# Kernel optimization log

Hardware: AMD Instinct MI355X
Metric: run time of the kernel (lower is better)

Reference implementation:

```python
import jax, jax.numpy as jnp
import numpy as np

EMBED = 256
HEADS = 8
HEAD_DIM = EMBED // HEADS
LEVELS = 4
POINTS = 4
QUERY_DIM = 128
NQ = QUERY_DIM * QUERY_DIM
HIDDEN = 512
CHANNELS = [24, 40, 112, 1280]
SHAPES = [(64, 64), (32, 32), (16, 16), (8, 8)]
EPS = 1e-5


def group_norm(x, g, b, groups=32, eps=EPS):
    B, C, H, W = x.shape
    xr = x.reshape(B, groups, C // groups, H, W)
    mu = xr.mean(axis=(2, 3, 4), keepdims=True)
    var = xr.var(axis=(2, 3, 4), keepdims=True)
    xn = ((xr - mu) / jnp.sqrt(var + eps)).reshape(B, C, H, W)
    return xn * g[:, None, None] + b[:, None, None]


def layer_norm(x, g, b, eps=EPS):
    mu = x.mean(-1, keepdims=True)
    var = x.var(-1, keepdims=True)
    return (x - mu) / jnp.sqrt(var + eps) * g + b


def _sample_level(v, loc):
    # v: (B, H8, hd, H, W) value for one level; loc: (B, nq, H8, P, 2) in [0,1]
    B, Hh, hd, H, W = v.shape
    nq, P = loc.shape[1], loc.shape[3]
    # grid_sample semantics, align_corners=False, zero padding
    x = loc[..., 0] * W - 0.5
    y = loc[..., 1] * H - 0.5
    x0 = jnp.floor(x)
    y0 = jnp.floor(y)
    dx = x - x0
    dy = y - y0
    x0i = x0.astype(jnp.int32)
    y0i = y0.astype(jnp.int32)
    vflat = v.reshape(B, Hh, hd, H * W)

    def gather(xi, yi):
        valid = ((xi >= 0) & (xi < W) & (yi >= 0) & (yi < H)).astype(v.dtype)
        idx = jnp.clip(yi, 0, H - 1) * W + jnp.clip(xi, 0, W - 1)
        idxr = idx.transpose(0, 2, 1, 3).reshape(B, Hh, 1, nq * P)
        g = jnp.take_along_axis(vflat, idxr, axis=3).reshape(B, Hh, hd, nq, P)
        return g * valid.transpose(0, 2, 1, 3)[:, :, None]

    g00 = gather(x0i, y0i)
    g01 = gather(x0i + 1, y0i)
    g10 = gather(x0i, y0i + 1)
    g11 = gather(x0i + 1, y0i + 1)
    wx = dx.transpose(0, 2, 1, 3)[:, :, None]  # (B,H8,1,nq,P)
    wy = dy.transpose(0, 2, 1, 3)[:, :, None]
    return g00 * (1 - wx) * (1 - wy) + g01 * wx * (1 - wy) + g10 * (1 - wx) * wy + g11 * wx * wy


def reference(Q, grd0, grd1, grd2, grd3, batch_size,
              proj_w0, proj_b0, gn_g0, gn_b0,
              proj_w1, proj_b1, gn_g1, gn_b1,
              proj_w2, proj_b2, gn_g2, gn_b2,
              proj_w3, proj_b3, gn_g3, gn_b3,
              value_w, value_b, off_w, off_b, attw_w, attw_b,
              out_w, out_b, lin1_w, lin1_b, lin2_w, lin2_b, ln_g, ln_b):
    grd = [grd0, grd1, grd2, grd3]
    proj_w = [proj_w0, proj_w1, proj_w2, proj_w3]
    proj_b = [proj_b0, proj_b1, proj_b2, proj_b3]
    gn_g = [gn_g0, gn_g1, gn_g2, gn_g3]
    gn_b = [gn_b0, gn_b1, gn_b2, gn_b3]

    B = Q.shape[0]
    # project each level to embed dims (1x1 conv + GroupNorm) and flatten
    feats = []
    for l in range(LEVELS):
        f = jnp.einsum('bchw,co->bohw', grd[l], proj_w[l]) + proj_b[l][:, None, None]
        f = group_norm(f, gn_g[l], gn_b[l])
        feats.append(f.reshape(B, EMBED, -1).transpose(0, 2, 1))  # (B, H*W, E)
    value = jnp.concatenate(feats, axis=1)  # (B, NV, E)

    # reference points: meshgrid 'xy' over linspace(0,1,query_dim), shape (1,nq,1,2)
    lin = jnp.linspace(0.0, 1.0, QUERY_DIM)
    gx, gy = jnp.meshgrid(lin, lin, indexing='xy')
    ref = jnp.stack([gx, gy], axis=-1).reshape(1, NQ, 1, 2)

    # MSDeformAttn (mmcv): value proj, sampling offsets, attention weights
    v = (value @ value_w + value_b).reshape(B, -1, HEADS, HEAD_DIM)
    offs = (Q @ off_w + off_b).reshape(B, NQ, HEADS, LEVELS, POINTS, 2)
    aw = (Q @ attw_w + attw_b).reshape(B, NQ, HEADS, LEVELS * POINTS)
    aw = jax.nn.softmax(aw, axis=-1).reshape(B, NQ, HEADS, LEVELS, POINTS)

    # offset normalizer: (W, H) per level
    norm = jnp.array([[w, h] for (h, w) in SHAPES], dtype=Q.dtype)  # (L,2)
    # sampling_locations: (B,nq,H8,L,P,2); ref broadcasts over heads/levels/points
    loc = ref[:, :, None, :, None, :] + offs / norm[None, None, None, :, None, :]

    starts = np.concatenate([[0], np.cumsum([h * w for h, w in SHAPES])])
    out = jnp.zeros((B, HEADS, HEAD_DIM, NQ), dtype=Q.dtype)
    for l, (H, W) in enumerate(SHAPES):
        vl = v[:, starts[l]:starts[l + 1]].transpose(0, 2, 3, 1).reshape(B, HEADS, HEAD_DIM, H, W)
        sampled = _sample_level(vl, loc[:, :, :, l])  # (B,H8,hd,nq,P)
        out = out + jnp.einsum('bhdqp,bqhp->bhdq', sampled, aw[:, :, :, l])
    attn = out.transpose(0, 3, 1, 2).reshape(B, NQ, EMBED)
    attn = attn @ out_w + out_b
    attn = attn + Q  # mmcv internal residual (dropout is identity in eval)

    fused = attn + Q
    ffn = layer_norm(jax.nn.relu(fused @ lin1_w + lin1_b) @ lin2_w + lin2_b, ln_g, ln_b)
    return fused + ffn


def setup_inputs() -> dict:
    key = jax.random.key(0)
    ks = jax.random.split(key, 40)
    B = 4
    d = {
        'Q': jax.random.normal(ks[0], (B, NQ, EMBED), jnp.float32),
        'grd0': jax.random.normal(ks[1], (B, 24, 64, 64), jnp.float32),
        'grd1': jax.random.normal(ks[2], (B, 40, 32, 32), jnp.float32),
        'grd2': jax.random.normal(ks[3], (B, 112, 16, 16), jnp.float32),
        'grd3': jax.random.normal(ks[4], (B, 1280, 8, 8), jnp.float32),
        'batch_size': B,
    }
    i = 5
    for l, c in enumerate(CHANNELS):
        d[f'proj_w{l}'] = jax.random.normal(ks[i], (c, EMBED), jnp.float32) * (1.0 / np.sqrt(c)); i += 1
        d[f'proj_b{l}'] = jnp.zeros((EMBED,), jnp.float32)
        d[f'gn_g{l}'] = jnp.ones((EMBED,), jnp.float32)
        d[f'gn_b{l}'] = jnp.zeros((EMBED,), jnp.float32)

    def lin(k, fin, fout, scale=1.0):
        return jax.random.normal(k, (fin, fout), jnp.float32) * (scale / np.sqrt(fin))

    d['value_w'] = lin(ks[i], EMBED, EMBED); i += 1
    d['value_b'] = jnp.zeros((EMBED,), jnp.float32)
    d['off_w'] = lin(ks[i], EMBED, HEADS * LEVELS * POINTS * 2, 0.1); i += 1
    d['off_b'] = jnp.zeros((HEADS * LEVELS * POINTS * 2,), jnp.float32)
    d['attw_w'] = lin(ks[i], EMBED, HEADS * LEVELS * POINTS); i += 1
    d['attw_b'] = jnp.zeros((HEADS * LEVELS * POINTS,), jnp.float32)
    d['out_w'] = lin(ks[i], EMBED, EMBED); i += 1
    d['out_b'] = jnp.zeros((EMBED,), jnp.float32)
    d['lin1_w'] = lin(ks[i], EMBED, HIDDEN); i += 1
    d['lin1_b'] = jnp.zeros((HIDDEN,), jnp.float32)
    d['lin2_w'] = lin(ks[i], HIDDEN, EMBED); i += 1
    d['lin2_b'] = jnp.zeros((EMBED,), jnp.float32)
    d['ln_g'] = jnp.ones((EMBED,), jnp.float32)
    d['ln_b'] = jnp.zeros((EMBED,), jnp.float32)
    return d
```

## Files before the change

### kernel.cpp

```cpp
#include <hip/hip_runtime.h>
#include <hip/hip_bf16.h>


#define NQc 16384
#define NVc 5440

typedef __attribute__((ext_vector_type(8))) short short8;
typedef __attribute__((ext_vector_type(4))) short short4v;
typedef __attribute__((ext_vector_type(4))) float f32x4;

#define GLOAD16(gp, lp)                                                        \
  __builtin_amdgcn_global_load_lds(                                           \
      (const __attribute__((address_space(1))) unsigned int*)(gp),            \
      (__attribute__((address_space(3))) unsigned int*)(lp), 16, 0, 0)

__device__ __forceinline__ float wred(float v) {
#pragma unroll
  for (int o = 32; o > 0; o >>= 1) v += __shfl_down(v, o);
  return v;
}

__global__ __launch_bounds__(256) void tcast_kernel(
    const float* __restrict__ w, __hip_bfloat16* __restrict__ wt, int K, int N) {
  int i = blockIdx.x * 256 + threadIdx.x;
  if (i < K * N) {
    int k = i / N, n = i - k * N;
    wt[(size_t)n * K + k] = __float2bfloat16(w[i]);
  }
}

__global__ __launch_bounds__(256) void tcast_pad_kernel(
    const float* __restrict__ w, __hip_bfloat16* __restrict__ wt,
    int K, int Kp, int N) {
  int i = blockIdx.x * 256 + threadIdx.x;
  if (i < N * Kp) {
    int n = i / Kp, k = i - n * Kp;
    wt[i] = (k < K) ? __float2bfloat16(w[k * N + n]) : __float2bfloat16(0.f);
  }
}

__global__ __launch_bounds__(256) void tpad_kernel(
    const float* __restrict__ grd, __hip_bfloat16* __restrict__ xp,
    int C, int Kp, int HW, int total) {
  const int i = blockIdx.x * 256 + threadIdx.x;
  if (i >= total) return;
  const int row = i / Kp;
  const int k = i - row * Kp;
  const int b = row / HW;
  const int hw = row - b * HW;
  xp[i] = (k < C) ? __float2bfloat16(grd[((size_t)b * C + k) * HW + hw])
                  : __float2bfloat16(0.f);
}

__global__ __launch_bounds__(256) void gn_kernel(
    const float* __restrict__ val, __hip_bfloat16* __restrict__ valb,
    const float* __restrict__ gg0, const float* __restrict__ gb0,
    const float* __restrict__ gg1, const float* __restrict__ gb1,
    const float* __restrict__ gg2, const float* __restrict__ gb2,
    const float* __restrict__ gg3, const float* __restrict__ gb3) {
  const int bid = blockIdx.x;
  const int grp = bid & 31;
  const int l = (bid >> 5) & 3;
  const int b = bid >> 7;
  int HW, startB; const float *gg, *gbeta;
  if (l == 0)      { HW = 4096; startB = 0;     gg = gg0; gbeta = gb0; }
  else if (l == 1) { HW = 1024; startB = 16384; gg = gg1; gbeta = gb1; }
  else if (l == 2) { HW = 256;  startB = 20480; gg = gg2; gbeta = gb2; }
  else             { HW = 64;   startB = 21504; gg = gg3; gbeta = gb3; }
  const int n = HW * 8;
  const size_t base = ((size_t)(startB + b * HW)) * 256 + grp * 8;
  float s = 0.f, s2 = 0.f;
  for (int i = threadIdx.x; i < n; i += 256) {
    float x = val[base + (size_t)(i >> 3) * 256 + (i & 7)];
    s += x; s2 += x * x;
  }
  s = wred(s); s2 = wred(s2);
  __shared__ float red[8];
  const int wv = threadIdx.x >> 6;
  if ((threadIdx.x & 63) == 0) { red[wv] = s; red[4 + wv] = s2; }
  __syncthreads();
  const float S = red[0] + red[1] + red[2] + red[3];
  const float S2 = red[4] + red[5] + red[6] + red[7];
  const float inv_n = 1.f / (float)n;
  const float mu = S * inv_n;
  const float var = S2 * inv_n - mu * mu;
  const float rstd = rsqrtf(var + 1e-5f);
  for (int i = threadIdx.x; i < n; i += 256) {
    const int j = i & 7;
    const int e = grp * 8 + j;
    const size_t idx = base + (size_t)(i >> 3) * 256 + j;
    const float y = (val[idx] - mu) * rstd * gg[e] + gbeta[e];
    valb[idx] = __float2bfloat16(y);
  }
}

template <int MODE, bool XF32>
__global__ __launch_bounds__(256) void gemm_bt(
    const void* __restrict__ Xv, const __hip_bfloat16* __restrict__ Wt,
    const float* __restrict__ bias, float* __restrict__ Cf,
    __hip_bfloat16* __restrict__ Cb, const float* __restrict__ Qres,
    int M, int N, int K) {
  const int m0 = blockIdx.x * 128;
  const int n0 = blockIdx.y * 128;
  const int tid = threadIdx.x;
  const int wave = tid >> 6;
  const int lane = tid & 63;
  const int wm = wave >> 1;
  const int wn = wave & 1;
  const int l15 = lane & 15;
  const int l4 = lane >> 4;
  __shared__ __align__(16) __hip_bfloat16 As[128 * 64];
  __shared__ __align__(16) __hip_bfloat16 Bs[128 * 64];
  f32x4 acc[4][4];
#pragma unroll
  for (int m = 0; m < 4; ++m)
#pragma unroll
    for (int n = 0; n < 4; ++n) acc[m][n] = (f32x4){0.f, 0.f, 0.f, 0.f};

  for (int k0 = 0; k0 < K; k0 += 64) {
#pragma unroll
    for (int j = 0; j < 4; ++j) {
      const int e = (j * 256 + tid) * 8;
      const int r = e >> 6;
      const int k = e & 63;
      if constexpr (XF32) {
        const float* Xf = (const float*)Xv;
        const float4 a = *reinterpret_cast<const float4*>(&Xf[(size_t)(m0 + r) * K + k0 + k]);
        const float4 b = *reinterpret_cast<const float4*>(&Xf[(size_t)(m0 + r) * K + k0 + k + 4]);
        union { __hip_bfloat16 h[8]; short8 v; } u;
        u.h[0] = __float2bfloat16(a.x); u.h[1] = __float2bfloat16(a.y);
        u.h[2] = __float2bfloat16(a.z); u.h[3] = __float2bfloat16(a.w);
        u.h[4] = __float2bfloat16(b.x); u.h[5] = __float2bfloat16(b.y);
        u.h[6] = __float2bfloat16(b.z); u.h[7] = __float2bfloat16(b.w);
        *reinterpret_cast<short8*>(&As[e]) = u.v;
        *reinterpret_cast<short8*>(&Bs[e]) =
            *reinterpret_cast<const short8*>(&Wt[(size_t)(n0 + r) * K + k0 + k]);
      } else {
        const __hip_bfloat16* Xb = (const __hip_bfloat16*)Xv;
        GLOAD16(&Xb[(size_t)(m0 + r) * K + k0 + k], &As[e]);
        GLOAD16(&Wt[(size_t)(n0 + r) * K + k0 + k], &Bs[e]);
      }
    }
    __syncthreads();
#pragma unroll
    for (int ks = 0; ks < 2; ++ks) {
      short8 a[4], bfr[4];
#pragma unroll
      for (int m = 0; m < 4; ++m)
        a[m] = *reinterpret_cast<const short8*>(
            &As[(wm * 64 + m * 16 + l15) * 64 + ks * 32 + l4 * 8]);
#pragma unroll
      for (int n = 0; n < 4; ++n)
        bfr[n] = *reinterpret_cast<const short8*>(
            &Bs[(wn * 64 + n * 16 + l15) * 64 + ks * 32 + l4 * 8]);
#pragma unroll
      for (int m = 0; m < 4; ++m)
#pragma unroll
        for (int n = 0; n < 4; ++n)
          acc[m][n] = __builtin_amdgcn_mfma_f32_16x16x32_bf16(a[m], bfr[n], acc[m][n], 0, 0, 0);
    }
    __syncthreads();
  }

#pragma unroll
  for (int m = 0; m < 4; ++m) {
    const int row0 = m0 + wm * 64 + m * 16 + l4 * 4;
#pragma unroll
    for (int n = 0; n < 4; ++n) {
      const int col = n0 + wn * 64 + n * 16 + l15;
      const float bv = bias[col];
#pragma unroll
      for (int r = 0; r < 4; ++r) {
        const size_t ci = (size_t)(row0 + r) * N + col;
        float f = acc[m][n][r] + bv;
        if (MODE == 0) {
          Cf[ci] = f;
        } else if (MODE == 1) {
          Cb[ci] = __float2bfloat16(fmaxf(f, 0.f));
        } else if (MODE == 2) {
          f += 2.f * Qres[ci];
          Cf[ci] = f;
          Cb[ci] = __float2bfloat16(f);
        } else {
          Cb[ci] = __float2bfloat16(f);
        }
      }
    }
  }
}

__global__ __launch_bounds__(256) void softmax_kernel(float* __restrict__ aw) {
  const size_t t = (size_t)blockIdx.x * 256 + threadIdx.x;
  float* p = aw + t * 16;
  float v[16];
  *reinterpret_cast<float4*>(&v[0])  = *reinterpret_cast<const float4*>(p + 0);
  *reinterpret_cast<float4*>(&v[4])  = *reinterpret_cast<const float4*>(p + 4);
  *reinterpret_cast<float4*>(&v[8])  = *reinterpret_cast<const float4*>(p + 8);
  *reinterpret_cast<float4*>(&v[12]) = *reinterpret_cast<const float4*>(p + 12);
  float mx = v[0];
#pragma unroll
  for (int j = 1; j < 16; ++j) mx = fmaxf(mx, v[j]);
  float sum = 0.f;
#pragma unroll
  for (int j = 0; j < 16; ++j) { v[j] = __expf(v[j] - mx); sum += v[j]; }
  const float inv = 1.f / sum;
#pragma unroll
  for (int j = 0; j < 16; ++j) v[j] *= inv;
  *reinterpret_cast<float4*>(p + 0)  = *reinterpret_cast<const float4*>(&v[0]);
  *reinterpret_cast<float4*>(p + 4)  = *reinterpret_cast<const float4*>(&v[4]);
  *reinterpret_cast<float4*>(p + 8)  = *reinterpret_cast<const float4*>(&v[8]);
  *reinterpret_cast<float4*>(p + 12) = *reinterpret_cast<const float4*>(&v[12]);
}

__global__ __launch_bounds__(256) void sampler_kernel(
    const float* __restrict__ V, const float* __restrict__ OFFS,
    const float* __restrict__ AW, __hip_bfloat16* __restrict__ ATT) {
  __shared__ int   sIdx[512 * 4];
  __shared__ float sW[512 * 4];
  const int blk = blockIdx.x;
  const int b = blk >> 12;
  const int q0 = (blk & 4095) << 2;
  const int bid0 = blk << 2;

  for (int j = threadIdx.x; j < 512; j += 256) {
    const int q   = j >> 7;
    const int h   = (j >> 4) & 7;
    const int tap = j & 15;
    const int l = tap >> 2;
    const int gq = bid0 + q;
    const int qq = q0 + q;
    const float rx = (float)(qq & 127) * (1.f / 127.f);
    const float ry = (float)(qq >> 7) * (1.f / 127.f);
    const float2 oxy = *reinterpret_cast<const float2*>(
        &OFFS[(size_t)gq * 256 + h * 32 + tap * 2]);
    const float aw = AW[(size_t)gq * 128 + h * 16 + tap];
    const int W = 64 >> l;
    const int HWl = W * W;
    const int startB = (l == 0) ? 0 : (l == 1) ? 16384 : (l == 2) ? 20480 : 21504;
    const int rowbase = startB + b * HWl;
    const float fW = (float)W;
    const float x = rx * fW + oxy.x - 0.5f;
    const float y = ry * fW + oxy.y - 0.5f;
    const float x0f = floorf(x);
    const float y0f = floorf(y);
    const int x0 = (int)x0f;
    const int y0 = (int)y0f;
    const float dx = x - x0f;
    const float dy = y - y0f;
    const int x1 = x0 + 1, y1 = y0 + 1;
    const float mx0 = (x0 >= 0 && x0 < W) ? 1.f : 0.f;
    const float mx1 = (x1 >= 0 && x1 < W) ? 1.f : 0.f;
    const float my0 = (y0 >= 0 && y0 < W) ? 1.f : 0.f;
    const float my1 = (y1 >= 0 && y1 < W) ? 1.f : 0.f;
    const int x0c = min(max(x0, 0), W - 1);
    const int x1c = min(max(x1, 0), W - 1);
    const int y0c = min(max(y0, 0), W - 1);
    const int y1c = min(max(y1, 0), W - 1);
    int4 I;
    I.x = rowbase + y0c * W + x0c;
    I.y = rowbase + y0c * W + x1c;
    I.z = rowbase + y1c * W + x0c;
    I.w = rowbase + y1c * W + x1c;
    float4 Wv;
    Wv.x = aw * (1.f - dx) * (1.f - dy) * (mx0 * my0);
    Wv.y = aw * dx * (1.f - dy) * (mx1 * my0);
    Wv.z = aw * (1.f - dx) * dy * (mx0 * my1);
    Wv.w = aw * dx * dy * (mx1 * my1);
    const int pj = (j & ~15) | (tap ^ h);
    *reinterpret_cast<int4*>(&sIdx[pj * 4]) = I;
    *reinterpret_cast<float4*>(&sW[pj * 4]) = Wv;
  }
  __syncthreads();

  const int q  = threadIdx.x >> 6;
  const int h  = (threadIdx.x >> 3) & 7;
  const int dq = threadIdx.x & 7;
  const float* vb = V + h * 32 + dq * 4;
  const int jbase = (q * 8 + h) * 16;
  f32x4 acc = (f32x4){0.f, 0.f, 0.f, 0.f};
#pragma unroll
  for (int tap = 0; tap < 16; ++tap) {
    const int pj = jbase + (tap ^ h);
    const int4   I  = *reinterpret_cast<const int4*>(&sIdx[pj * 4]);
    const float4 Wv = *reinterpret_cast<const float4*>(&sW[pj * 4]);
    const f32x4 v00 = *reinterpret_cast<const f32x4*>(vb + ((size_t)I.x << 8));
    const f32x4 v01 = *reinterpret_cast<const f32x4*>(vb + ((size_t)I.y << 8));
    const f32x4 v10 = *reinterpret_cast<const f32x4*>(vb + ((size_t)I.z << 8));
    const f32x4 v11 = *reinterpret_cast<const f32x4*>(vb + ((size_t)I.w << 8));
    acc += v00 * Wv.x;
    acc += v01 * Wv.y;
    acc += v10 * Wv.z;
    acc += v11 * Wv.w;
  }
  union { __hip_bfloat16 hh[4]; short4v v; } u;
  u.hh[0] = __float2bfloat16(acc.x);
  u.hh[1] = __float2bfloat16(acc.y);
  u.hh[2] = __float2bfloat16(acc.z);
  u.hh[3] = __float2bfloat16(acc.w);
  *reinterpret_cast<short4v*>(
      &ATT[(size_t)(bid0 + q) * 256 + h * 32 + dq * 4]) = u.v;
}

__global__ __launch_bounds__(256) void ln_add_kernel(
    const __hip_bfloat16* __restrict__ T, const float* __restrict__ lng,
    const float* __restrict__ lnb, float* __restrict__ out) {
  const size_t row = blockIdx.x;
  const int e = threadIdx.x;
  const float t = __bfloat162float(T[row * 256 + e]);
  float s = wred(t);
  float s2 = wred(t * t);
  __shared__ float red[8];
  const int wv = e >> 6;
  if ((e & 63) == 0) { red[wv] = s; red[4 + wv] = s2; }
  __syncthreads();
  const float S = red[0] + red[1] + red[2] + red[3];
  const float S2 = red[4] + red[5] + red[6] + red[7];
  const float mu = S * (1.f / 256.f);
  const float var = S2 * (1.f / 256.f) - mu * mu;
  const float y = (t - mu) * rsqrtf(var + 1e-5f) * lng[e] + lnb[e];
  out[row * 256 + e] += y;
}

extern "C" void kernel_launch(void* const* d_in, const int* in_sizes, int n_in,
                              void* d_out, int out_size, void* d_ws, size_t ws_size,
                              hipStream_t stream) {
  const float* Q  = (const float*)d_in[0];
  const float* g0 = (const float*)d_in[1];
  const float* g1 = (const float*)d_in[2];
  const float* g2 = (const float*)d_in[3];
  const float* g3 = (const float*)d_in[4];
  const float* pw0 = (const float*)d_in[6];
  const float* pb0 = (const float*)d_in[7];
  const float* gg0 = (const float*)d_in[8];
  const float* gb0 = (const float*)d_in[9];
  const float* pw1 = (const float*)d_in[10];
  const float* pb1 = (const float*)d_in[11];
  const float* gg1 = (const float*)d_in[12];
  const float* gb1 = (const float*)d_in[13];
  const float* pw2 = (const float*)d_in[14];
  const float* pb2 = (const float*)d_in[15];
  const float* gg2 = (const float*)d_in[16];
  const float* gb2 = (const float*)d_in[17];
  const float* pw3 = (const float*)d_in[18];
  const float* pb3 = (const float*)d_in[19];
  const float* gg3 = (const float*)d_in[20];
  const float* gb3 = (const float*)d_in[21];
  const float* value_w = (const float*)d_in[22];
  const float* value_b = (const float*)d_in[23];
  const float* off_w   = (const float*)d_in[24];
  const float* off_b   = (const float*)d_in[25];
  const float* attw_w  = (const float*)d_in[26];
  const float* attw_b  = (const float*)d_in[27];
  const float* out_w   = (const float*)d_in[28];
  const float* out_b   = (const float*)d_in[29];
  const float* lin1_w  = (const float*)d_in[30];
  const float* lin1_b  = (const float*)d_in[31];
  const float* lin2_w  = (const float*)d_in[32];
  const float* lin2_b  = (const float*)d_in[33];
  const float* ln_g    = (const float*)d_in[34];
  const float* ln_b    = (const float*)d_in[35];

  char* ws = (char*)d_ws;
  __hip_bfloat16* WT_VALUE = (__hip_bfloat16*)(ws + 0);
  __hip_bfloat16* WT_OFF   = (__hip_bfloat16*)(ws + 131072);
  __hip_bfloat16* WT_ATTW  = (__hip_bfloat16*)(ws + 262144);
  __hip_bfloat16* WT_OUT   = (__hip_bfloat16*)(ws + 327680);
  __hip_bfloat16* WT_LIN1  = (__hip_bfloat16*)(ws + 458752);
  __hip_bfloat16* WT_LIN2  = (__hip_bfloat16*)(ws + 720896);
  __hip_bfloat16* WTP0     = (__hip_bfloat16*)(ws + 983040);
  __hip_bfloat16* WTP1     = (__hip_bfloat16*)(ws + 1015808);
  __hip_bfloat16* WTP2     = (__hip_bfloat16*)(ws + 1048576);
  __hip_bfloat16* WTP3     = (__hip_bfloat16*)(ws + 1114112);
  __hip_bfloat16* XP0      = (__hip_bfloat16*)(ws + 1769472);
  __hip_bfloat16* XP1      = (__hip_bfloat16*)(ws + 3866624);
  __hip_bfloat16* XP2      = (__hip_bfloat16*)(ws + 4390912);
  __hip_bfloat16* XP3      = (__hip_bfloat16*)(ws + 4653056);
  float*          VAL      = (float*)(ws + 34406400);
  __hip_bfloat16* VALB     = (__hip_bfloat16*)(ws + 23265280);
  float*          V        = (float*)(ws + 983040);
  float*          AW       = (float*)(ws + 23265280);
  __hip_bfloat16* ATT      = (__hip_bfloat16*)(ws + 56819712);
  __hip_bfloat16* FUSEDB   = (__hip_bfloat16*)(ws + 983040);
  __hip_bfloat16* HIDH     = (__hip_bfloat16*)(ws + 34537472);
  __hip_bfloat16* T16H     = (__hip_bfloat16*)(ws + 68091904);
  float*          OFFS     = (float*)d_out;
  float*          FUSED    = (float*)d_out;

  tcast_kernel<<<256, 256, 0, stream>>>(value_w, WT_VALUE, 256, 256);
  tcast_kernel<<<256, 256, 0, stream>>>(off_w,   WT_OFF,   256, 256);
  tcast_kernel<<<128, 256, 0, stream>>>(attw_w,  WT_ATTW,  256, 128);
  tcast_kernel<<<256, 256, 0, stream>>>(out_w,   WT_OUT,   256, 256);
  tcast_kernel<<<512, 256, 0, stream>>>(lin1_w,  WT_LIN1,  256, 512);
  tcast_kernel<<<512, 256, 0, stream>>>(lin2_w,  WT_LIN2,  512, 256);
  tcast_pad_kernel<<<64,   256, 0, stream>>>(pw0, WTP0, 24,   64,   256);
  tcast_pad_kernel<<<64,   256, 0, stream>>>(pw1, WTP1, 40,   64,   256);
  tcast_pad_kernel<<<128,  256, 0, stream>>>(pw2, WTP2, 112,  128,  256);
  tcast_pad_kernel<<<1280, 256, 0, stream>>>(pw3, WTP3, 1280, 1280, 256);

  tpad_kernel<<<4096, 256, 0, stream>>>(g0, XP0, 24,   64,   4096, 16384 * 64);
  tpad_kernel<<<1024, 256, 0, stream>>>(g1, XP1, 40,   64,   1024, 4096 * 64);
  tpad_kernel<<<512,  256, 0, stream>>>(g2, XP2, 112,  128,  256,  1024 * 128);
  tpad_kernel<<<1280, 256, 0, stream>>>(g3, XP3, 1280, 1280, 64,   256 * 1280);

  gemm_bt<0, false><<<dim3(128, 2), 256, 0, stream>>>(XP0, WTP0, pb0, VAL,
                                                      nullptr, nullptr, 16384, 256, 64);
  gemm_bt<0, false><<<dim3(32, 2), 256, 0, stream>>>(XP1, WTP1, pb1, VAL + (size_t)16384 * 256,
                                                     nullptr, nullptr, 4096, 256, 64);
  gemm_bt<0, false><<<dim3(8, 2), 256, 0, stream>>>(XP2, WTP2, pb2, VAL + (size_t)20480 * 256,
                                                    nullptr, nullptr, 1024, 256, 128);
  gemm_bt<0, false><<<dim3(2, 2), 256, 0, stream>>>(XP3, WTP3, pb3, VAL + (size_t)21504 * 256,
                                                    nullptr, nullptr, 256, 256, 1280);
  gn_kernel<<<512, 256, 0, stream>>>(VAL, VALB, gg0, gb0, gg1, gb1, gg2, gb2, gg3, gb3);
  gemm_bt<0, false><<<dim3(170, 2), 256, 0, stream>>>(VALB, WT_VALUE, value_b, V,
                                                      nullptr, nullptr, 21760, 256, 256);

  gemm_bt<0, true><<<dim3(512, 2), 256, 0, stream>>>(Q, WT_OFF, off_b, OFFS,
                                                     nullptr, nullptr, 65536, 256, 256);
  gemm_bt<0, true><<<dim3(512, 1), 256, 0, stream>>>(Q, WT_ATTW, attw_b, AW,
                                                     nullptr, nullptr, 65536, 128, 256);
  softmax_kernel<<<2048, 256, 0, stream>>>(AW);

  sampler_kernel<<<16384, 256, 0, stream>>>(V, OFFS, AW, ATT);

  gemm_bt<2, false><<<dim3(512, 2), 256, 0, stream>>>(ATT, WT_OUT, out_b, FUSED,
                                                      FUSEDB, Q, 65536, 256, 256);

  for (int h = 0; h < 2; ++h) {
    const __hip_bfloat16* Xh = FUSEDB + (size_t)h * 32768 * 256;
    gemm_bt<1, false><<<dim3(256, 4), 256, 0, stream>>>(Xh, WT_LIN1, lin1_b, nullptr,
                                                        HIDH, nullptr, 32768, 512, 256);
    gemm_bt<3, false><<<dim3(256, 2), 256, 0, stream>>>(HIDH, WT_LIN2, lin2_b, nullptr,
                                                        T16H, nullptr, 32768, 256, 512);
    ln_add_kernel<<<32768, 256, 0, stream>>>(T16H, ln_g, ln_b,
                                             FUSED + (size_t)h * 32768 * 256);
  }
}
```

Baseline: 680.7 us.

## Merge prep kernels, fuse softmax into sampler, store value tensor in bf16

Replaces the ten weight-transpose launches with one segmented prep kernel and the four input-pad launches with one kernel, which cuts launch overhead. Removes the standalone softmax pass over the attention weights by doing a 16-lane shuffle softmax inside the sampler. The value projection now writes bf16 instead of fp32, so the sampler's gathers read half as many bytes. The trade-off is lower precision in the sampled values and some extra shuffle work in the sampler setup.

```diff
diff --git a/kernel.cpp b/kernel.cpp
--- a/kernel.cpp
+++ b/kernel.cpp
@@ -20,36 +20,64 @@
   return v;
 }
 
-__global__ __launch_bounds__(256) void tcast_kernel(
-    const float* __restrict__ w, __hip_bfloat16* __restrict__ wt, int K, int N) {
-  int i = blockIdx.x * 256 + threadIdx.x;
-  if (i < K * N) {
-    int k = i / N, n = i - k * N;
-    wt[(size_t)n * K + k] = __float2bfloat16(w[i]);
-  }
-}
-
-__global__ __launch_bounds__(256) void tcast_pad_kernel(
-    const float* __restrict__ w, __hip_bfloat16* __restrict__ wt,
-    int K, int Kp, int N) {
-  int i = blockIdx.x * 256 + threadIdx.x;
-  if (i < N * Kp) {
-    int n = i / Kp, k = i - n * Kp;
-    wt[i] = (k < K) ? __float2bfloat16(w[k * N + n]) : __float2bfloat16(0.f);
-  }
-}
-
-__global__ __launch_bounds__(256) void tpad_kernel(
-    const float* __restrict__ grd, __hip_bfloat16* __restrict__ xp,
-    int C, int Kp, int HW, int total) {
+__device__ __forceinline__ float b2f(unsigned short u) {
+  union { unsigned int i; float f; } c;
+  c.i = ((unsigned int)u) << 16;
+  return c.f;
+}
+
+__global__ __launch_bounds__(256) void prep_kernel(
+    const float* s0, const float* s1, const float* s2, const float* s3,
+    const float* s4, const float* s5, const float* s6, const float* s7,
+    const float* s8, const float* s9,
+    __hip_bfloat16* d0, __hip_bfloat16* d1, __hip_bfloat16* d2,
+    __hip_bfloat16* d3, __hip_bfloat16* d4, __hip_bfloat16* d5,
+    __hip_bfloat16* d6, __hip_bfloat16* d7, __hip_bfloat16* d8,
+    __hip_bfloat16* d9) {
   const int i = blockIdx.x * 256 + threadIdx.x;
-  if (i >= total) return;
-  const int row = i / Kp;
-  const int k = i - row * Kp;
-  const int b = row / HW;
-  const int hw = row - b * HW;
-  xp[i] = (k < C) ? __float2bfloat16(grd[((size_t)b * C + k) * HW + hw])
-                  : __float2bfloat16(0.f);
+#define SEG(lo, hi, K, Kp, N, src, dst)                                        \
+  if (i < (hi)) {                                                              \
+    const int j = i - (lo);                                                    \
+    const int n = j / (Kp), k = j - n * (Kp);                                  \
+    dst[j] = (k < (K)) ? __float2bfloat16(src[k * (N) + n])                    \
+                       : __float2bfloat16(0.f);                                \
+    return;                                                                    \
+  }
+  SEG(0,      65536,  256,  256,  256, s0, d0)
+  SEG(65536,  131072, 256,  256,  256, s1, d1)
+  SEG(131072, 163840, 256,  256,  128, s2, d2)
+  SEG(163840, 229376, 256,  256,  256, s3, d3)
+  SEG(229376, 360448, 256,  256,  512, s4, d4)
+  SEG(360448, 491520, 512,  512,  256, s5, d5)
+  SEG(491520, 507904, 24,   64,   256, s6, d6)
+  SEG(507904, 524288, 40,   64,   256, s7, d7)
+  SEG(524288, 557056, 112,  128,  256, s8, d8)
+  SEG(557056, 884736, 1280, 1280, 256, s9, d9)
+#undef SEG
+}
+
+__global__ __launch_bounds__(256) void tpad_all_kernel(
+    const float* g0, const float* g1, const float* g2, const float* g3,
+    __hip_bfloat16* x0, __hip_bfloat16* x1, __hip_bfloat16* x2,
+    __hip_bfloat16* x3) {
+  const int i = blockIdx.x * 256 + threadIdx.x;
+#define TSEG(lo, hi, C, Kp, HW, src, dst)                                      \
+  if (i < (hi)) {                                                              \
+    const int j = i - (lo);                                                    \
+    const int row = j / (Kp);                                                  \
+    const int k = j - row * (Kp);                                              \
+    const int b = row / (HW);                                                  \
+    const int hw = row - b * (HW);                                             \
+    dst[j] = (k < (C))                                                         \
+        ? __float2bfloat16(src[((size_t)b * (C) + k) * (HW) + hw])             \
+        : __float2bfloat16(0.f);                                               \
+    return;                                                                    \
+  }
+  TSEG(0,       1048576, 24,   64,   4096, g0, x0)
+  TSEG(1048576, 1310720, 40,   64,   1024, g1, x1)
+  TSEG(1310720, 1441792, 112,  128,  256,  g2, x2)
+  TSEG(1441792, 1769472, 1280, 1280, 64,   g3, x3)
+#undef TSEG
 }
 
 __global__ __launch_bounds__(256) void gn_kernel(
@@ -189,32 +217,9 @@
   }
 }
 
-__global__ __launch_bounds__(256) void softmax_kernel(float* __restrict__ aw) {
-  const size_t t = (size_t)blockIdx.x * 256 + threadIdx.x;
-  float* p = aw + t * 16;
-  float v[16];
-  *reinterpret_cast<float4*>(&v[0])  = *reinterpret_cast<const float4*>(p + 0);
-  *reinterpret_cast<float4*>(&v[4])  = *reinterpret_cast<const float4*>(p + 4);
-  *reinterpret_cast<float4*>(&v[8])  = *reinterpret_cast<const float4*>(p + 8);
-  *reinterpret_cast<float4*>(&v[12]) = *reinterpret_cast<const float4*>(p + 12);
-  float mx = v[0];
-#pragma unroll
-  for (int j = 1; j < 16; ++j) mx = fmaxf(mx, v[j]);
-  float sum = 0.f;
-#pragma unroll
-  for (int j = 0; j < 16; ++j) { v[j] = __expf(v[j] - mx); sum += v[j]; }
-  const float inv = 1.f / sum;
-#pragma unroll
-  for (int j = 0; j < 16; ++j) v[j] *= inv;
-  *reinterpret_cast<float4*>(p + 0)  = *reinterpret_cast<const float4*>(&v[0]);
-  *reinterpret_cast<float4*>(p + 4)  = *reinterpret_cast<const float4*>(&v[4]);
-  *reinterpret_cast<float4*>(p + 8)  = *reinterpret_cast<const float4*>(&v[8]);
-  *reinterpret_cast<float4*>(p + 12) = *reinterpret_cast<const float4*>(&v[12]);
-}
-
 __global__ __launch_bounds__(256) void sampler_kernel(
-    const float* __restrict__ V, const float* __restrict__ OFFS,
-    const float* __restrict__ AW, __hip_bfloat16* __restrict__ ATT) {
+    const __hip_bfloat16* __restrict__ VB, const float* __restrict__ OFFS,
+    const float* __restrict__ AWr, __hip_bfloat16* __restrict__ ATT) {
   __shared__ int   sIdx[512 * 4];
   __shared__ float sW[512 * 4];
   const int blk = blockIdx.x;
@@ -233,7 +238,16 @@
     const float ry = (float)(qq >> 7) * (1.f / 127.f);
     const float2 oxy = *reinterpret_cast<const float2*>(
         &OFFS[(size_t)gq * 256 + h * 32 + tap * 2]);
-    const float aw = AW[(size_t)gq * 128 + h * 16 + tap];
+    const float s_raw = AWr[(size_t)gq * 128 + h * 16 + tap];
+    float mx = s_raw;
+#pragma unroll
+    for (int o = 1; o < 16; o <<= 1) mx = fmaxf(mx, __shfl_xor(mx, o));
+    const float ex = __expf(s_raw - mx);
+    float sum = ex;
+#pragma unroll
+    for (int o = 1; o < 16; o <<= 1) sum += __shfl_xor(sum, o);
+    const float aw = ex / sum;
+
     const int W = 64 >> l;
     const int HWl = W * W;
     const int startB = (l == 0) ? 0 : (l == 1) ? 16384 : (l == 2) ? 20480 : 21504;
@@ -275,7 +289,7 @@
   const int q  = threadIdx.x >> 6;
   const int h  = (threadIdx.x >> 3) & 7;
   const int dq = threadIdx.x & 7;
-  const float* vb = V + h * 32 + dq * 4;
+  const __hip_bfloat16* vb = VB + h * 32 + dq * 4;
   const int jbase = (q * 8 + h) * 16;
   f32x4 acc = (f32x4){0.f, 0.f, 0.f, 0.f};
 #pragma unroll
@@ -283,20 +297,23 @@
     const int pj = jbase + (tap ^ h);
     const int4   I  = *reinterpret_cast<const int4*>(&sIdx[pj * 4]);
     const float4 Wv = *reinterpret_cast<const float4*>(&sW[pj * 4]);
-    const f32x4 v00 = *reinterpret_cast<const f32x4*>(vb + ((size_t)I.x << 8));
-    const f32x4 v01 = *reinterpret_cast<const f32x4*>(vb + ((size_t)I.y << 8));
-    const f32x4 v10 = *reinterpret_cast<const f32x4*>(vb + ((size_t)I.z << 8));
-    const f32x4 v11 = *reinterpret_cast<const f32x4*>(vb + ((size_t)I.w << 8));
-    acc += v00 * Wv.x;
-    acc += v01 * Wv.y;
-    acc += v10 * Wv.z;
-    acc += v11 * Wv.w;
+    const short4v r00 = *reinterpret_cast<const short4v*>(vb + ((size_t)I.x << 8));
+    const short4v r01 = *reinterpret_cast<const short4v*>(vb + ((size_t)I.y << 8));
+    const short4v r10 = *reinterpret_cast<const short4v*>(vb + ((size_t)I.z << 8));
+    const short4v r11 = *reinterpret_cast<const short4v*>(vb + ((size_t)I.w << 8));
+#pragma unroll
+    for (int d = 0; d < 4; ++d) {
+      acc[d] += b2f((unsigned short)r00[d]) * Wv.x +
+                b2f((unsigned short)r01[d]) * Wv.y +
+                b2f((unsigned short)r10[d]) * Wv.z +
+                b2f((unsigned short)r11[d]) * Wv.w;
+    }
   }
   union { __hip_bfloat16 hh[4]; short4v v; } u;
-  u.hh[0] = __float2bfloat16(acc.x);
-  u.hh[1] = __float2bfloat16(acc.y);
-  u.hh[2] = __float2bfloat16(acc.z);
-  u.hh[3] = __float2bfloat16(acc.w);
+  u.hh[0] = __float2bfloat16(acc[0]);
+  u.hh[1] = __float2bfloat16(acc[1]);
+  u.hh[2] = __float2bfloat16(acc[2]);
+  u.hh[3] = __float2bfloat16(acc[3]);
   *reinterpret_cast<short4v*>(
       &ATT[(size_t)(bid0 + q) * 256 + h * 32 + dq * 4]) = u.v;
 }
@@ -377,8 +394,8 @@
   __hip_bfloat16* XP3      = (__hip_bfloat16*)(ws + 4653056);
   float*          VAL      = (float*)(ws + 34406400);
   __hip_bfloat16* VALB     = (__hip_bfloat16*)(ws + 23265280);
-  float*          V        = (float*)(ws + 983040);
-  float*          AW       = (float*)(ws + 23265280);
+  __hip_bfloat16* VB       = (__hip_bfloat16*)(ws + 983040);
+  float*          AWr      = (float*)(ws + 23265280);
   __hip_bfloat16* ATT      = (__hip_bfloat16*)(ws + 56819712);
   __hip_bfloat16* FUSEDB   = (__hip_bfloat16*)(ws + 983040);
   __hip_bfloat16* HIDH     = (__hip_bfloat16*)(ws + 34537472);
@@ -386,21 +403,12 @@
   float*          OFFS     = (float*)d_out;
   float*          FUSED    = (float*)d_out;
 
-  tcast_kernel<<<256, 256, 0, stream>>>(value_w, WT_VALUE, 256, 256);
-  tcast_kernel<<<256, 256, 0, stream>>>(off_w,   WT_OFF,   256, 256);
-  tcast_kernel<<<128, 256, 0, stream>>>(attw_w,  WT_ATTW,  256, 128);
-  tcast_kernel<<<256, 256, 0, stream>>>(out_w,   WT_OUT,   256, 256);
-  tcast_kernel<<<512, 256, 0, stream>>>(lin1_w,  WT_LIN1,  256, 512);
-  tcast_kernel<<<512, 256, 0, stream>>>(lin2_w,  WT_LIN2,  512, 256);
-  tcast_pad_kernel<<<64,   256, 0, stream>>>(pw0, WTP0, 24,   64,   256);
-  tcast_pad_kernel<<<64,   256, 0, stream>>>(pw1, WTP1, 40,   64,   256);
-  tcast_pad_kernel<<<128,  256, 0, stream>>>(pw2, WTP2, 112,  128,  256);
-  tcast_pad_kernel<<<1280, 256, 0, stream>>>(pw3, WTP3, 1280, 1280, 256);
-
-  tpad_kernel<<<4096, 256, 0, stream>>>(g0, XP0, 24,   64,   4096, 16384 * 64);
-  tpad_kernel<<<1024, 256, 0, stream>>>(g1, XP1, 40,   64,   1024, 4096 * 64);
-  tpad_kernel<<<512,  256, 0, stream>>>(g2, XP2, 112,  128,  256,  1024 * 128);
-  tpad_kernel<<<1280, 256, 0, stream>>>(g3, XP3, 1280, 1280, 64,   256 * 1280);
+  prep_kernel<<<3456, 256, 0, stream>>>(value_w, off_w, attw_w, out_w, lin1_w,
+                                        lin2_w, pw0, pw1, pw2, pw3,
+                                        WT_VALUE, WT_OFF, WT_ATTW, WT_OUT,
+                                        WT_LIN1, WT_LIN2, WTP0, WTP1, WTP2, WTP3);
+
+  tpad_all_kernel<<<6912, 256, 0, stream>>>(g0, g1, g2, g3, XP0, XP1, XP2, XP3);
 
   gemm_bt<0, false><<<dim3(128, 2), 256, 0, stream>>>(XP0, WTP0, pb0, VAL,
                                                       nullptr, nullptr, 16384, 256, 64);
@@ -411,16 +419,15 @@
   gemm_bt<0, false><<<dim3(2, 2), 256, 0, stream>>>(XP3, WTP3, pb3, VAL + (size_t)21504 * 256,
                                                     nullptr, nullptr, 256, 256, 1280);
   gn_kernel<<<512, 256, 0, stream>>>(VAL, VALB, gg0, gb0, gg1, gb1, gg2, gb2, gg3, gb3);
-  gemm_bt<0, false><<<dim3(170, 2), 256, 0, stream>>>(VALB, WT_VALUE, value_b, V,
-                                                      nullptr, nullptr, 21760, 256, 256);
+  gemm_bt<3, false><<<dim3(170, 2), 256, 0, stream>>>(VALB, WT_VALUE, value_b, nullptr,
+                                                      VB, nullptr, 21760, 256, 256);
 
   gemm_bt<0, true><<<dim3(512, 2), 256, 0, stream>>>(Q, WT_OFF, off_b, OFFS,
                                                      nullptr, nullptr, 65536, 256, 256);
-  gemm_bt<0, true><<<dim3(512, 1), 256, 0, stream>>>(Q, WT_ATTW, attw_b, AW,
+  gemm_bt<0, true><<<dim3(512, 1), 256, 0, stream>>>(Q, WT_ATTW, attw_b, AWr,
                                                      nullptr, nullptr, 65536, 128, 256);
-  softmax_kernel<<<2048, 256, 0, stream>>>(AW);
-
-  sampler_kernel<<<16384, 256, 0, stream>>>(V, OFFS, AW, ATT);
+
+  sampler_kernel<<<16384, 256, 0, stream>>>(VB, OFFS, AWr, ATT);
 
   gemm_bt<2, false><<<dim3(512, 2), 256, 0, stream>>>(ATT, WT_OUT, out_b, FUSED,
                                                       FUSEDB, Q, 65536, 256, 256);
```

New measurement: 669.0 us. Within noise of the previous version (-1.7%).
